# Kernel optimization log

Measured on AMD Instinct MI355X. Metric: run time of the kernel, lower is better.

Reference implementation:

```python
import jax, jax.numpy as jnp
import numpy as np

N, D, E, H, K = 8192, 1024, 8, 256, 2


def setup_inputs() -> dict:
    key = jax.random.key(0)
    ks = jax.random.split(key, 9)
    s = 0.02
    return {
        "x": jax.random.normal(ks[0], (N, D), dtype=jnp.float32),
        "Wg": jax.random.normal(ks[1], (D, E), dtype=jnp.float32) * s,
        "bg": jnp.zeros((E,), dtype=jnp.float32),
        "W1": jax.random.normal(ks[2], (E, D, H), dtype=jnp.float32) * s,
        "b1": jnp.zeros((E, H), dtype=jnp.float32),
        "W2": jax.random.normal(ks[3], (E, H, H), dtype=jnp.float32) * s,
        "b2": jnp.zeros((E, H), dtype=jnp.float32),
        "W3": jax.random.normal(ks[4], (E, H, D), dtype=jnp.float32) * s,
        "b3": jnp.zeros((E, D), dtype=jnp.float32),
    }


def reference(x, Wg, bg, W1, b1, W2, b2, W3, b3):
    # Gating: softmax over experts, then keep only top-k gate values per token.
    gates = jax.nn.softmax(x @ Wg + bg, axis=-1)              # [N, E]
    top_v, top_i = jax.lax.top_k(gates, K)                    # [N, K]
    rows = jnp.arange(gates.shape[0])[:, None]                # [N, 1]
    top_k_gates = jnp.zeros_like(gates).at[rows, top_i].set(top_v)  # [N, E]

    # Dense all-expert MLP (matches original: every expert runs on every token).
    h = jax.nn.relu(jnp.einsum('nd,edh->neh', x, W1) + b1)    # [N, E, H]
    h = jax.nn.relu(jnp.einsum('neh,ehg->neg', h, W2) + b2)   # [N, E, H]  (dropout is eval no-op)
    eo = jax.nn.relu(jnp.einsum('neh,ehd->ned', h, W3) + b3)  # [N, E, D]

    # Combine with masked gates: einsum('...nde,...ne->...nd') with eo in 'ned' layout.
    output = jnp.einsum('ned,ne->nd', eo, top_k_gates)        # [N, D]
    return output
```

## Files before the change

### kernel.cpp

```cpp
#include <hip/hip_runtime.h>
#include <math.h>

#define NTOK 8192
#define DDIM 1024
#define NEXP 8
#define HDIM 256
#define TOPK 2
#define PADM 128
#define CAPS (NTOK * TOPK + NEXP * PADM)
#define NT64  (CAPS / 64)
#define NT128 (CAPS / 128)

typedef __attribute__((ext_vector_type(8))) __bf16 bf16x8;
typedef __attribute__((ext_vector_type(4))) float f32x4;

#define GLDS16(g, s)                                                      \
    __builtin_amdgcn_global_load_lds(                                     \
        (const __attribute__((address_space(1))) void*)(g),               \
        (__attribute__((address_space(3))) void*)(s), 16, 0, 0)

static constexpr size_t OFF_TOFF = 128;
static constexpr size_t OFF_ZBUF = 4096;
static constexpr size_t OFF_T2E  = 8192;
static constexpr size_t OFF_T2G  = OFF_T2E + (size_t)NTOK * TOPK * 4;
static constexpr size_t OFF_SLOT = OFF_T2G + (size_t)NTOK * TOPK * 4;
static constexpr size_t OFF_TOK  = OFF_SLOT + (size_t)NTOK * TOPK * 4;
static constexpr size_t OFF_GAT  = OFF_TOK + (size_t)CAPS * 4;
static constexpr size_t OFF_XB   = (OFF_GAT + (size_t)CAPS * 4 + 255) & ~(size_t)255;
static constexpr size_t OFF_W1T  = OFF_XB  + (size_t)NTOK * DDIM * 2;
static constexpr size_t OFF_W2T  = OFF_W1T + (size_t)NEXP * DDIM * HDIM * 2;
static constexpr size_t OFF_W3T  = OFF_W2T + (size_t)NEXP * HDIM * HDIM * 2;
static constexpr size_t OFF_H2   = OFF_W3T + (size_t)NEXP * HDIM * DDIM * 2;
static constexpr size_t OFF_H3   = OFF_H2  + (size_t)CAPS * HDIM * 2;

static __device__ __forceinline__ unsigned short f2b(float f) {
    __bf16 h = (__bf16)f;
    return __builtin_bit_cast(unsigned short, h);
}
static __device__ __forceinline__ float b2f(unsigned short u) {
    return __builtin_bit_cast(float, ((unsigned)u) << 16);
}

__global__ __launch_bounds__(256) void gate_trans(
    const float* __restrict__ x, const float* __restrict__ Wg,
    const float* __restrict__ bg, unsigned short* __restrict__ xb,
    int* __restrict__ top2e, float* __restrict__ top2g,
    const float* __restrict__ W1, const float* __restrict__ W2,
    const float* __restrict__ W3, __bf16* __restrict__ w1t,
    __bf16* __restrict__ w2t, __bf16* __restrict__ w3t)
{
    __shared__ __align__(16) float sh[NEXP * DDIM];
    const int tid = threadIdx.x;

    if (blockIdx.x < 256) {
        for (int d = tid; d < DDIM; d += 256) {
            const float4 w0 = *(const float4*)(Wg + (size_t)d * NEXP);
            const float4 w1 = *(const float4*)(Wg + (size_t)d * NEXP + 4);
            sh[0 * DDIM + d] = w0.x; sh[1 * DDIM + d] = w0.y;
            sh[2 * DDIM + d] = w0.z; sh[3 * DDIM + d] = w0.w;
            sh[4 * DDIM + d] = w1.x; sh[5 * DDIM + d] = w1.y;
            sh[6 * DDIM + d] = w1.z; sh[7 * DDIM + d] = w1.w;
        }
        __syncthreads();

        const int n = (blockIdx.y * 256 + blockIdx.x) * 4 + (tid >> 6);
        const int lane = tid & 63;
        const float* xr = x + (size_t)n * DDIM;
        unsigned short* xbr = xb + (size_t)n * DDIM;

        float acc[NEXP];
#pragma unroll
        for (int e = 0; e < NEXP; ++e) acc[e] = 0.f;

#pragma unroll
        for (int it = 0; it < 4; ++it) {
            const int d = it * 256 + lane * 4;
            const float4 xv = *(const float4*)(xr + d);
            ushort4 u;
            u.x = f2b(xv.x); u.y = f2b(xv.y); u.z = f2b(xv.z); u.w = f2b(xv.w);
            *(ushort4*)(xbr + d) = u;
#pragma unroll
            for (int e = 0; e < NEXP; ++e) {
                const float4 wt = *(const float4*)(sh + e * DDIM + d);
                acc[e] = fmaf(xv.x, wt.x, acc[e]);
                acc[e] = fmaf(xv.y, wt.y, acc[e]);
                acc[e] = fmaf(xv.z, wt.z, acc[e]);
                acc[e] = fmaf(xv.w, wt.w, acc[e]);
            }
        }
#pragma unroll
        for (int off = 32; off > 0; off >>= 1)
#pragma unroll
            for (int e = 0; e < NEXP; ++e) acc[e] += __shfl_down(acc[e], off, 64);

        if (lane == 0) {
            float v[NEXP], mx = -1e30f;
#pragma unroll
            for (int e = 0; e < NEXP; ++e) { v[e] = acc[e] + bg[e]; mx = fmaxf(mx, v[e]); }
            float p[NEXP], s = 0.f;
#pragma unroll
            for (int e = 0; e < NEXP; ++e) { p[e] = expf(v[e] - mx); s += p[e]; }
            const float inv = 1.f / s;
#pragma unroll
            for (int e = 0; e < NEXP; ++e) p[e] *= inv;
            int i0 = 0;
#pragma unroll
            for (int e = 1; e < NEXP; ++e) if (p[e] > p[i0]) i0 = e;
            int i1 = (i0 == 0) ? 1 : 0;
#pragma unroll
            for (int e = 0; e < NEXP; ++e) if (e != i0 && p[e] > p[i1]) i1 = e;
            top2e[n * 2 + 0] = i0;  top2e[n * 2 + 1] = i1;
            top2g[n * 2 + 0] = p[i0]; top2g[n * 2 + 1] = p[i1];
        }
    } else {
        const int e = blockIdx.y;
        int bt = blockIdx.x - 256;
        const float* Wi; __bf16* Wo; int R, C, xt, yt;
        if (bt < 256)      { Wi = W1; Wo = w1t; R = DDIM; C = HDIM; xt = bt & 7;  yt = bt >> 3; }
        else if (bt < 320) { bt -= 256; Wi = W2; Wo = w2t; R = HDIM; C = HDIM; xt = bt & 7;  yt = bt >> 3; }
        else               { bt -= 320; Wi = W3; Wo = w3t; R = HDIM; C = DDIM; xt = bt & 31; yt = bt >> 5; }
        const int r0 = yt * 32, c0 = xt * 32;
        const int tx = tid & 31, ty = tid >> 5;
        const float* Wie = Wi + (size_t)e * R * C;
        __bf16* Woe = Wo + (size_t)e * C * R;
#pragma unroll
        for (int j = 0; j < 4; ++j)
            sh[(ty + j * 8) * 33 + tx] = Wie[(size_t)(r0 + ty + j * 8) * C + c0 + tx];
        __syncthreads();
#pragma unroll
        for (int j = 0; j < 4; ++j)
            Woe[(size_t)(c0 + ty + j * 8) * R + r0 + tx] = (__bf16)sh[tx * 33 + ty + j * 8];
    }
}

__global__ __launch_bounds__(1024) void route(
    const int* __restrict__ top2e, const float* __restrict__ top2g,
    int* __restrict__ toff, int* __restrict__ tok, float* __restrict__ gat,
    int* __restrict__ slotof, float* __restrict__ zbuf)
{
    const int tid = threadIdx.x;
    const int wv = tid >> 6, ln = tid & 63;
    __shared__ int   waveTot[16][NEXP];
    __shared__ int   waveBase[16][NEXP];
    __shared__ int   totS[NEXP];
    __shared__ int   toffS[NEXP + 1];
    __shared__ short excS[1024][NEXP];

    zbuf[tid] = 0.f;

    int myE[16]; float myG[16];
    const int4*   pe = (const int4*)(top2e + tid * 16);
    const float4* pg = (const float4*)(top2g + tid * 16);
#pragma unroll
    for (int q = 0; q < 4; ++q) {
        const int4 v = pe[q];
        myE[q * 4 + 0] = v.x; myE[q * 4 + 1] = v.y;
        myE[q * 4 + 2] = v.z; myE[q * 4 + 3] = v.w;
        const float4 g = pg[q];
        myG[q * 4 + 0] = g.x; myG[q * 4 + 1] = g.y;
        myG[q * 4 + 2] = g.z; myG[q * 4 + 3] = g.w;
    }

#pragma unroll
    for (int e = 0; e < NEXP; ++e) {
        int c = 0;
#pragma unroll
        for (int j = 0; j < 16; ++j) c += (myE[j] == e);
        int inc = c;
#pragma unroll
        for (int off = 1; off < 64; off <<= 1) {
            const int t = __shfl_up(inc, off, 64);
            if (ln >= off) inc += t;
        }
        excS[tid][e] = (short)(inc - c);
        if (ln == 63) waveTot[wv][e] = inc;
    }
    __syncthreads();

    if (tid < NEXP) {
        int b = 0;
#pragma unroll
        for (int w = 0; w < 16; ++w) {
            const int t = waveTot[w][tid];
            waveBase[w][tid] = b;
            b += t;
        }
        totS[tid] = b;
    }
    __syncthreads();

    if (tid == 0) {
        int acc = 0;
#pragma unroll
        for (int e = 0; e < NEXP; ++e) {
            toffS[e] = acc;
            acc += (totS[e] + PADM - 1) & ~(PADM - 1);
        }
        toffS[NEXP] = acc;
#pragma unroll
        for (int e = 0; e <= NEXP; ++e) toff[e] = toffS[e];
    }
    __syncthreads();

#pragma unroll
    for (int j = 0; j < 16; ++j) {
        int pre = 0;
#pragma unroll
        for (int j2 = 0; j2 < j; ++j2) pre += (myE[j2] == myE[j]);
        const int e = myE[j];
        const int slot = toffS[e] + waveBase[wv][e] + (int)excS[tid][e] + pre;
        const int i = tid * 16 + j;
        tok[slot] = i >> 1;
        gat[slot] = myG[j];
        slotof[i] = slot;
    }

#pragma unroll
    for (int e = 0; e < NEXP; ++e) {
        const int begin = toffS[e] + totS[e];
        const int end   = toffS[e + 1];
        for (int i = begin + tid; i < end; i += 1024) {
            tok[i] = -1;
            gat[i] = 0.f;
        }
    }
}

__global__ __launch_bounds__(256) void egemm12(
    const __bf16* __restrict__ xb, const __bf16* __restrict__ w1t,
    const __bf16* __restrict__ w2t, const float* __restrict__ b1,
    const float* __restrict__ b2, const int* __restrict__ toff,
    const int* __restrict__ tok, const char* __restrict__ zbuf,
    __bf16* __restrict__ h2)
{
    const int total = toff[NEXP];
    const int slot0 = blockIdx.x * 64;
    if (slot0 >= total) return;
    int e = 0;
    while (toff[e + 1] <= slot0) ++e;

    __shared__ __align__(16) char smem[73728];
    char* AsB = smem;
    char* BsB = smem + 8192;
    char* H1s = smem + 40960;

    const int tid  = threadIdx.x;
    const int lane = tid & 63;
    const int wid  = tid >> 6;

    const int srow  = tid >> 3;
    const int sslot = tid & 7;
    const int ks    = sslot ^ (srow & 7);

    const __bf16* We1 = w1t + (size_t)e * HDIM * DDIM;
    const char* ap[2];
#pragma unroll
    for (int i = 0; i < 2; ++i) {
        const int t = tok[slot0 + i * 32 + srow];
        ap[i] = (t >= 0) ? (const char*)(xb + (size_t)t * DDIM + ks * 8)
                         : (const char*)zbuf;
    }
    const char* bp1[8];
#pragma unroll
    for (int i = 0; i < 8; ++i)
        bp1[i] = (const char*)(We1 + (size_t)(i * 32 + srow) * DDIM + ks * 8);

    const int llo = lane & 15, lhi = lane >> 4;
    const int m7 = llo & 7;
    int abyte[4], bbyte[4];
#pragma unroll
    for (int m = 0; m < 4; ++m) {
        abyte[m] = (m * 16 + llo) * 128;
        bbyte[m] = (wid * 64 + m * 16 + llo) * 128;
    }

    f32x4 acc[4][4];
#pragma unroll
    for (int m = 0; m < 4; ++m)
#pragma unroll
        for (int n = 0; n < 4; ++n) acc[m][n] = (f32x4){0.f, 0.f, 0.f, 0.f};

    for (int k0 = 0; k0 < DDIM; k0 += 64) {
        const size_t kb = (size_t)k0 * 2;
        GLDS16(ap[0] + kb, AsB + tid * 16);
        GLDS16(ap[1] + kb, AsB + 4096 + tid * 16);
#pragma unroll
        for (int i = 0; i < 8; ++i)
            GLDS16(bp1[i] + kb, BsB + i * 4096 + tid * 16);
        __syncthreads();
#pragma unroll
        for (int kk = 0; kk < 2; ++kk) {
            const int sl = ((kk << 2) + lhi) ^ m7;
            bf16x8 af[4], bfr[4];
#pragma unroll
            for (int m = 0; m < 4; ++m) af[m]  = *(const bf16x8*)(AsB + abyte[m] + (sl << 4));
#pragma unroll
            for (int n = 0; n < 4; ++n) bfr[n] = *(const bf16x8*)(BsB + bbyte[n] + (sl << 4));
#pragma unroll
            for (int m = 0; m < 4; ++m)
#pragma unroll
                for (int n = 0; n < 4; ++n)
                    acc[m][n] = __builtin_amdgcn_mfma_f32_16x16x32_bf16(
                        af[m], bfr[n], acc[m][n], 0, 0, 0);
        }
        __syncthreads();
    }

    {
        const float* be1 = b1 + (size_t)e * HDIM;
#pragma unroll
        for (int n = 0; n < 4; ++n) {
            const int col = wid * 64 + n * 16 + llo;
            const float bb = be1[col];
            const int colbyte = (col & 7) * 2;
            const int slice = col >> 3;
#pragma unroll
            for (int m = 0; m < 4; ++m) {
#pragma unroll
                for (int j = 0; j < 4; ++j) {
                    const int r = m * 16 + lhi * 4 + j;
                    const float v = fmaxf(acc[m][n][j] + bb, 0.f);
                    *(__bf16*)(H1s + r * 512 + ((slice ^ (r & 7)) << 4) + colbyte) = (__bf16)v;
                }
                acc[m][n] = (f32x4){0.f, 0.f, 0.f, 0.f};
            }
        }
    }
    __syncthreads();

    const __bf16* We2 = w2t + (size_t)e * HDIM * HDIM;
    const char* bp2[8];
#pragma unroll
    for (int i = 0; i < 8; ++i)
        bp2[i] = (const char*)(We2 + (size_t)(i * 32 + srow) * HDIM + ks * 8);

    for (int k2 = 0; k2 < 4; ++k2) {
        const size_t kb = (size_t)k2 * 128;
#pragma unroll
        for (int i = 0; i < 8; ++i)
            GLDS16(bp2[i] + kb, BsB + i * 4096 + tid * 16);
        __syncthreads();
#pragma unroll
        for (int kk = 0; kk < 2; ++kk) {
            const int slB = ((kk << 2) + lhi) ^ m7;
            const int sA  = k2 * 8 + (kk << 2) + lhi;
            const int slA = sA ^ m7;
            bf16x8 af[4], bfr[4];
#pragma unroll
            for (int m = 0; m < 4; ++m)
                af[m] = *(const bf16x8*)(H1s + (m * 16 + llo) * 512 + (slA << 4));
#pragma unroll
            for (int n = 0; n < 4; ++n)
                bfr[n] = *(const bf16x8*)(BsB + bbyte[n] + (slB << 4));
#pragma unroll
            for (int m = 0; m < 4; ++m)
#pragma unroll
                for (int n = 0; n < 4; ++n)
                    acc[m][n] = __builtin_amdgcn_mfma_f32_16x16x32_bf16(
                        af[m], bfr[n], acc[m][n], 0, 0, 0);
        }
        __syncthreads();
    }

    {
        const float* be2 = b2 + (size_t)e * HDIM;
#pragma unroll
        for (int n = 0; n < 4; ++n) {
            const int col = wid * 64 + n * 16 + llo;
            const float bb = be2[col];
#pragma unroll
            for (int m = 0; m < 4; ++m) {
#pragma unroll
                for (int j = 0; j < 4; ++j) {
                    const int r = slot0 + m * 16 + lhi * 4 + j;
                    h2[(size_t)r * HDIM + col] = (__bf16)fmaxf(acc[m][n][j] + bb, 0.f);
                }
            }
        }
    }
}

template<int KDIM, int NCOL>
__global__ __launch_bounds__(256) void egemm3(
    const __bf16* __restrict__ Ain, const __bf16* __restrict__ Wt,
    const float* __restrict__ ball, const int* __restrict__ toff,
    const float* __restrict__ gat, __bf16* __restrict__ Out)
{
    const int total = toff[NEXP];
    const int slot0 = blockIdx.y * 128;
    if (slot0 >= total) return;
    int e = 0;
    while (toff[e + 1] <= slot0) ++e;
    const int col0 = blockIdx.x * 128;

    __shared__ __align__(16) char smem[32768];
    char* AsB = smem;
    char* BsB = smem + 16384;

    const int tid  = threadIdx.x;
    const int lane = tid & 63;
    const int wid  = tid >> 6;
    const int wr = wid >> 1, wc = wid & 1;

    const int srow  = tid >> 3;
    const int sslot = tid & 7;
    const int ks    = sslot ^ (srow & 7);
    const __bf16* We = Wt + (size_t)e * NCOL * KDIM;
    const char* ap[4];
    const char* bp[4];
#pragma unroll
    for (int i = 0; i < 4; ++i) {
        const int row = i * 32 + srow;
        ap[i] = (const char*)(Ain + (size_t)(slot0 + row) * KDIM + ks * 8);
        bp[i] = (const char*)(We + (size_t)(col0 + row) * KDIM + ks * 8);
    }

    const int llo = lane & 15, lhi = lane >> 4;
    const int m7 = llo & 7;
    int abyte[4], bbyte[4];
#pragma unroll
    for (int m = 0; m < 4; ++m) {
        abyte[m] = (wr * 64 + m * 16 + llo) * 128;
        bbyte[m] = (wc * 64 + m * 16 + llo) * 128;
    }

    f32x4 acc[4][4];
#pragma unroll
    for (int m = 0; m < 4; ++m)
#pragma unroll
        for (int n = 0; n < 4; ++n) acc[m][n] = (f32x4){0.f, 0.f, 0.f, 0.f};

    for (int k0 = 0; k0 < KDIM; k0 += 64) {
        const size_t kb = (size_t)k0 * 2;
#pragma unroll
        for (int i = 0; i < 4; ++i)
            GLDS16(ap[i] + kb, AsB + i * 4096 + wid * 1024);
#pragma unroll
        for (int i = 0; i < 4; ++i)
            GLDS16(bp[i] + kb, BsB + i * 4096 + wid * 1024);
        __syncthreads();
#pragma unroll
        for (int kk = 0; kk < 2; ++kk) {
            const int sl = ((kk << 2) + lhi) ^ m7;
            bf16x8 af[4], bfr[4];
#pragma unroll
            for (int m = 0; m < 4; ++m) af[m]  = *(const bf16x8*)(AsB + abyte[m] + (sl << 4));
#pragma unroll
            for (int n = 0; n < 4; ++n) bfr[n] = *(const bf16x8*)(BsB + bbyte[n] + (sl << 4));
#pragma unroll
            for (int m = 0; m < 4; ++m)
#pragma unroll
                for (int n = 0; n < 4; ++n)
                    acc[m][n] = __builtin_amdgcn_mfma_f32_16x16x32_bf16(
                        af[m], bfr[n], acc[m][n], 0, 0, 0);
        }
        __syncthreads();
    }

    const float* be = ball + (size_t)e * NCOL;
#pragma unroll
    for (int m = 0; m < 4; ++m) {
        const int rbase = slot0 + wr * 64 + m * 16 + lhi * 4;
        float g[4];
#pragma unroll
        for (int j = 0; j < 4; ++j) g[j] = gat[rbase + j];
#pragma unroll
        for (int n = 0; n < 4; ++n) {
            const int col = col0 + wc * 64 + n * 16 + llo;
            const float bb = be[col];
#pragma unroll
            for (int j = 0; j < 4; ++j) {
                const float v = fmaxf(acc[m][n][j] + bb, 0.f) * g[j];
                Out[(size_t)(rbase + j) * NCOL + col] = (__bf16)v;
            }
        }
    }
}

__global__ __launch_bounds__(256) void combine(
    const unsigned short* __restrict__ h3, const int* __restrict__ slotof,
    float* __restrict__ out)
{
    const int n = blockIdx.x;
    const int c = threadIdx.x * 4;
    const int s0 = slotof[n * 2], s1 = slotof[n * 2 + 1];
    const ushort4 a = *(const ushort4*)(h3 + (size_t)s0 * DDIM + c);
    const ushort4 b = *(const ushort4*)(h3 + (size_t)s1 * DDIM + c);
    float4 o;
    o.x = b2f(a.x) + b2f(b.x);
    o.y = b2f(a.y) + b2f(b.y);
    o.z = b2f(a.z) + b2f(b.z);
    o.w = b2f(a.w) + b2f(b.w);
    *(float4*)(out + (size_t)n * DDIM + c) = o;
}

extern "C" void kernel_launch(void* const* d_in, const int* in_sizes, int n_in,
                              void* d_out, int out_size, void* d_ws, size_t ws_size,
                              hipStream_t stream)
{
    const float* x  = (const float*)d_in[0];
    const float* Wg = (const float*)d_in[1];
    const float* bg = (const float*)d_in[2];
    const float* W1 = (const float*)d_in[3];
    const float* b1 = (const float*)d_in[4];
    const float* W2 = (const float*)d_in[5];
    const float* b2 = (const float*)d_in[6];
    const float* W3 = (const float*)d_in[7];
    const float* b3 = (const float*)d_in[8];
    float* out = (float*)d_out;

    char* ws = (char*)d_ws;
    int*   toff   = (int*)(ws + OFF_TOFF);
    char*  zbuf   = ws + OFF_ZBUF;
    int*   top2e  = (int*)(ws + OFF_T2E);
    float* top2g  = (float*)(ws + OFF_T2G);
    int*   slotof = (int*)(ws + OFF_SLOT);
    int*   tok    = (int*)(ws + OFF_TOK);
    float* gat    = (float*)(ws + OFF_GAT);
    unsigned short* xbu = (unsigned short*)(ws + OFF_XB);
    __bf16* xb  = (__bf16*)(ws + OFF_XB);
    __bf16* w1t = (__bf16*)(ws + OFF_W1T);
    __bf16* w2t = (__bf16*)(ws + OFF_W2T);
    __bf16* w3t = (__bf16*)(ws + OFF_W3T);
    __bf16* h2  = (__bf16*)(ws + OFF_H2);
    __bf16* h3  = (__bf16*)(ws + OFF_H3);

    gate_trans<<<dim3(832, NEXP), 256, 0, stream>>>(
        x, Wg, bg, xbu, top2e, top2g, W1, W2, W3, w1t, w2t, w3t);
    route<<<1, 1024, 0, stream>>>(top2e, top2g, toff, tok, gat, slotof, (float*)zbuf);

    egemm12<<<NT64, 256, 0, stream>>>(xb, w1t, w2t, b1, b2, toff, tok, zbuf, h2);
    egemm3<HDIM, DDIM><<<dim3(DDIM / 128, NT128), 256, 0, stream>>>(
        h2, w3t, b3, toff, gat, h3);

    combine<<<NTOK, 256, 0, stream>>>((const unsigned short*)h3, slotof, out);
}
```

Measured before the change: 106.5 us.

## Fuse third expert GEMM into the first two, keeping h2 in shared memory

Merges the separate third-layer GEMM kernel into the layer-1/2 kernel. The ReLU'd layer-2 output is written swizzled into shared memory and reused as the A operand for the W3 GEMM, looping over four 256-column chunks of the output. This removes the h2 round trip through global memory and one kernel launch. In exchange, each 64-row block now processes all 1024 output columns serially, which gives fewer and longer blocks with less parallelism for the third GEMM, and W3 is re-read by every block.

```diff
diff --git a/kernel.cpp b/kernel.cpp
--- a/kernel.cpp
+++ b/kernel.cpp
@@ -9,7 +9,6 @@
 #define PADM 128
 #define CAPS (NTOK * TOPK + NEXP * PADM)
 #define NT64  (CAPS / 64)
-#define NT128 (CAPS / 128)
 
 typedef __attribute__((ext_vector_type(8))) __bf16 bf16x8;
 typedef __attribute__((ext_vector_type(4))) float f32x4;
@@ -226,12 +225,13 @@
     }
 }
 
-__global__ __launch_bounds__(256) void egemm12(
+__global__ __launch_bounds__(256) void egemm123(
     const __bf16* __restrict__ xb, const __bf16* __restrict__ w1t,
-    const __bf16* __restrict__ w2t, const float* __restrict__ b1,
-    const float* __restrict__ b2, const int* __restrict__ toff,
-    const int* __restrict__ tok, const char* __restrict__ zbuf,
-    __bf16* __restrict__ h2)
+    const __bf16* __restrict__ w2t, const __bf16* __restrict__ w3t,
+    const float* __restrict__ b1, const float* __restrict__ b2,
+    const float* __restrict__ b3, const int* __restrict__ toff,
+    const int* __restrict__ tok, const float* __restrict__ gat,
+    const char* __restrict__ zbuf, __bf16* __restrict__ h3)
 {
     const int total = toff[NEXP];
     const int slot0 = blockIdx.x * 64;
@@ -368,110 +368,77 @@
         for (int n = 0; n < 4; ++n) {
             const int col = wid * 64 + n * 16 + llo;
             const float bb = be2[col];
+            const int colbyte = (col & 7) * 2;
+            const int slice = col >> 3;
 #pragma unroll
             for (int m = 0; m < 4; ++m) {
 #pragma unroll
                 for (int j = 0; j < 4; ++j) {
-                    const int r = slot0 + m * 16 + lhi * 4 + j;
-                    h2[(size_t)r * HDIM + col] = (__bf16)fmaxf(acc[m][n][j] + bb, 0.f);
+                    const int r = m * 16 + lhi * 4 + j;
+                    const float v = fmaxf(acc[m][n][j] + bb, 0.f);
+                    *(__bf16*)(H1s + r * 512 + ((slice ^ (r & 7)) << 4) + colbyte) = (__bf16)v;
                 }
             }
         }
     }
-}
-
-template<int KDIM, int NCOL>
-__global__ __launch_bounds__(256) void egemm3(
-    const __bf16* __restrict__ Ain, const __bf16* __restrict__ Wt,
-    const float* __restrict__ ball, const int* __restrict__ toff,
-    const float* __restrict__ gat, __bf16* __restrict__ Out)
-{
-    const int total = toff[NEXP];
-    const int slot0 = blockIdx.y * 128;
-    if (slot0 >= total) return;
-    int e = 0;
-    while (toff[e + 1] <= slot0) ++e;
-    const int col0 = blockIdx.x * 128;
-
-    __shared__ __align__(16) char smem[32768];
-    char* AsB = smem;
-    char* BsB = smem + 16384;
-
-    const int tid  = threadIdx.x;
-    const int lane = tid & 63;
-    const int wid  = tid >> 6;
-    const int wr = wid >> 1, wc = wid & 1;
-
-    const int srow  = tid >> 3;
-    const int sslot = tid & 7;
-    const int ks    = sslot ^ (srow & 7);
-    const __bf16* We = Wt + (size_t)e * NCOL * KDIM;
-    const char* ap[4];
-    const char* bp[4];
-#pragma unroll
-    for (int i = 0; i < 4; ++i) {
-        const int row = i * 32 + srow;
-        ap[i] = (const char*)(Ain + (size_t)(slot0 + row) * KDIM + ks * 8);
-        bp[i] = (const char*)(We + (size_t)(col0 + row) * KDIM + ks * 8);
-    }
-
-    const int llo = lane & 15, lhi = lane >> 4;
-    const int m7 = llo & 7;
-    int abyte[4], bbyte[4];
-#pragma unroll
-    for (int m = 0; m < 4; ++m) {
-        abyte[m] = (wr * 64 + m * 16 + llo) * 128;
-        bbyte[m] = (wc * 64 + m * 16 + llo) * 128;
-    }
-
-    f32x4 acc[4][4];
+    __syncthreads();
+
+    const __bf16* We3 = w3t + (size_t)e * DDIM * HDIM;
+    const float* be3 = b3 + (size_t)e * DDIM;
+    float gv[4][4];
 #pragma unroll
     for (int m = 0; m < 4; ++m)
 #pragma unroll
-        for (int n = 0; n < 4; ++n) acc[m][n] = (f32x4){0.f, 0.f, 0.f, 0.f};
-
-    for (int k0 = 0; k0 < KDIM; k0 += 64) {
-        const size_t kb = (size_t)k0 * 2;
-#pragma unroll
-        for (int i = 0; i < 4; ++i)
-            GLDS16(ap[i] + kb, AsB + i * 4096 + wid * 1024);
-#pragma unroll
-        for (int i = 0; i < 4; ++i)
-            GLDS16(bp[i] + kb, BsB + i * 4096 + wid * 1024);
-        __syncthreads();
-#pragma unroll
-        for (int kk = 0; kk < 2; ++kk) {
-            const int sl = ((kk << 2) + lhi) ^ m7;
-            bf16x8 af[4], bfr[4];
-#pragma unroll
-            for (int m = 0; m < 4; ++m) af[m]  = *(const bf16x8*)(AsB + abyte[m] + (sl << 4));
-#pragma unroll
-            for (int n = 0; n < 4; ++n) bfr[n] = *(const bf16x8*)(BsB + bbyte[n] + (sl << 4));
-#pragma unroll
-            for (int m = 0; m < 4; ++m)
+        for (int j = 0; j < 4; ++j)
+            gv[m][j] = gat[slot0 + m * 16 + lhi * 4 + j];
+
+    for (int cc = 0; cc < 4; ++cc) {
+#pragma unroll
+        for (int m = 0; m < 4; ++m)
+#pragma unroll
+            for (int n = 0; n < 4; ++n) acc[m][n] = (f32x4){0.f, 0.f, 0.f, 0.f};
+
+        for (int k2 = 0; k2 < 4; ++k2) {
+            const size_t kb = (size_t)k2 * 128;
+#pragma unroll
+            for (int i = 0; i < 8; ++i)
+                GLDS16((const char*)(We3 + (size_t)(cc * 256 + i * 32 + srow) * HDIM + ks * 8) + kb,
+                       BsB + i * 4096 + tid * 16);
+            __syncthreads();
+#pragma unroll
+            for (int kk = 0; kk < 2; ++kk) {
+                const int slB = ((kk << 2) + lhi) ^ m7;
+                const int sA  = k2 * 8 + (kk << 2) + lhi;
+                const int slA = sA ^ m7;
+                bf16x8 af[4], bfr[4];
+#pragma unroll
+                for (int m = 0; m < 4; ++m)
+                    af[m] = *(const bf16x8*)(H1s + (m * 16 + llo) * 512 + (slA << 4));
 #pragma unroll
                 for (int n = 0; n < 4; ++n)
-                    acc[m][n] = __builtin_amdgcn_mfma_f32_16x16x32_bf16(
-                        af[m], bfr[n], acc[m][n], 0, 0, 0);
-        }
-        __syncthreads();
-    }
-
-    const float* be = ball + (size_t)e * NCOL;
-#pragma unroll
-    for (int m = 0; m < 4; ++m) {
-        const int rbase = slot0 + wr * 64 + m * 16 + lhi * 4;
-        float g[4];
-#pragma unroll
-        for (int j = 0; j < 4; ++j) g[j] = gat[rbase + j];
-#pragma unroll
-        for (int n = 0; n < 4; ++n) {
-            const int col = col0 + wc * 64 + n * 16 + llo;
-            const float bb = be[col];
-#pragma unroll
-            for (int j = 0; j < 4; ++j) {
-                const float v = fmaxf(acc[m][n][j] + bb, 0.f) * g[j];
-                Out[(size_t)(rbase + j) * NCOL + col] = (__bf16)v;
+                    bfr[n] = *(const bf16x8*)(BsB + bbyte[n] + (slB << 4));
+#pragma unroll
+                for (int m = 0; m < 4; ++m)
+#pragma unroll
+                    for (int n = 0; n < 4; ++n)
+                        acc[m][n] = __builtin_amdgcn_mfma_f32_16x16x32_bf16(
+                            af[m], bfr[n], acc[m][n], 0, 0, 0);
+            }
+            __syncthreads();
+        }
+
+#pragma unroll
+        for (int m = 0; m < 4; ++m) {
+            const int rbase = slot0 + m * 16 + lhi * 4;
+#pragma unroll
+            for (int n = 0; n < 4; ++n) {
+                const int col = cc * 256 + wid * 64 + n * 16 + llo;
+                const float bb = be3[col];
+#pragma unroll
+                for (int j = 0; j < 4; ++j) {
+                    const float v = fmaxf(acc[m][n][j] + bb, 0.f) * gv[m][j];
+                    h3[(size_t)(rbase + j) * DDIM + col] = (__bf16)v;
+                }
             }
         }
     }
@@ -522,16 +489,14 @@
     __bf16* w1t = (__bf16*)(ws + OFF_W1T);
     __bf16* w2t = (__bf16*)(ws + OFF_W2T);
     __bf16* w3t = (__bf16*)(ws + OFF_W3T);
-    __bf16* h2  = (__bf16*)(ws + OFF_H2);
     __bf16* h3  = (__bf16*)(ws + OFF_H3);
 
     gate_trans<<<dim3(832, NEXP), 256, 0, stream>>>(
         x, Wg, bg, xbu, top2e, top2g, W1, W2, W3, w1t, w2t, w3t);
     route<<<1, 1024, 0, stream>>>(top2e, top2g, toff, tok, gat, slotof, (float*)zbuf);
 
-    egemm12<<<NT64, 256, 0, stream>>>(xb, w1t, w2t, b1, b2, toff, tok, zbuf, h2);
-    egemm3<HDIM, DDIM><<<dim3(DDIM / 128, NT128), 256, 0, stream>>>(
-        h2, w3t, b3, toff, gat, h3);
+    egemm123<<<NT64, 256, 0, stream>>>(xb, w1t, w2t, w3t, b1, b2, b3,
+                                       toff, tok, gat, zbuf, h3);
 
     combine<<<NTOK, 256, 0, stream>>>((const unsigned short*)h3, slotof, out);
 }
```

Result: slower. 112.0 us (+5.2%).
